# Optimization experiments

Hardware: AMD Instinct MI355X
Metric: run time of the kernel (lower is better)

## Reference

```python
import jax, jax.numpy as jnp
import numpy as np

T, H, I, E = 4096, 1024, 512, 16


def setup_inputs() -> dict:
    key = jax.random.key(0)
    k1, k2, k3 = jax.random.split(key, 3)
    x = jax.random.normal(k1, (T, H), dtype=jnp.float32)
    gate_up_proj = jax.random.normal(k2, (E, H, 2 * I), dtype=jnp.float32) * 0.02
    down_proj = jax.random.normal(k3, (E, I, H), dtype=jnp.float32) * 0.02
    # uneven expert token counts summing exactly to T (no padding rows)
    rng = np.random.default_rng(0)
    raw = rng.integers(64, 512, size=E)
    counts = (raw * T) // raw.sum()
    counts[-1] += T - counts.sum()
    num_tokens_per_expert = jnp.asarray(counts, dtype=jnp.int32)
    return {"x": x, "gate_up_proj": gate_up_proj, "down_proj": down_proj,
            "num_tokens_per_expert": num_tokens_per_expert}


def reference(x, gate_up_proj, down_proj, num_tokens_per_expert):
    # tokens are sorted by expert; build per-token expert id (jit-safe: fixed length)
    n_tok = x.shape[0]
    n_exp = gate_up_proj.shape[0]
    seg = jnp.repeat(jnp.arange(n_exp), num_tokens_per_expert, total_repeat_length=n_tok)  # [T]

    def body(acc, ew):
        e, w_gu, w_d = ew
        xe = jnp.where((seg == e)[:, None], x, jnp.zeros((), x.dtype))  # [T, H], zero rows for other experts
        gu = xe @ w_gu                                                  # [T, 2I]
        g, u = jnp.split(gu, 2, axis=-1)
        o = (jax.nn.silu(g) * u) @ w_d                                  # [T, H]; masked rows stay exactly 0
        return acc + o, None

    init = jnp.zeros((n_tok, down_proj.shape[-1]), x.dtype)
    out, _ = jax.lax.scan(body, init, (jnp.arange(n_exp), gate_up_proj, down_proj))
    return out
```

## Files before the change

### kernel.cpp

```cpp
#include <hip/hip_runtime.h>

#define H_DIM 1024
#define I_DIM 512
#define E_EXP 16
#define BM    128
#define BK    64

using bf16x8   = __attribute__((ext_vector_type(8))) short;
using floatx4  = __attribute__((ext_vector_type(4))) float;
using ushort4v = __attribute__((ext_vector_type(4))) unsigned short;

__device__ __forceinline__ unsigned short f2bf(float f) {
  union { float f; unsigned u; } v; v.f = f;
  return (unsigned short)((v.u + 0x7FFFu + ((v.u >> 16) & 1u)) >> 16);
}
__device__ __forceinline__ unsigned pk2(float a, float b) {
  return (unsigned)f2bf(a) | ((unsigned)f2bf(b) << 16);
}

__device__ __forceinline__ void gld16(const void* g, void* l) {
  __builtin_amdgcn_global_load_lds((const __attribute__((address_space(1))) void*)g,
                                   (__attribute__((address_space(3))) void*)l,
                                   16, 0, 0);
}

__device__ __forceinline__ void bar_lgkm() {
  asm volatile("s_waitcnt lgkmcnt(0)" ::: "memory");
  __builtin_amdgcn_sched_barrier(0);
  __builtin_amdgcn_s_barrier();
  __builtin_amdgcn_sched_barrier(0);
}
__device__ __forceinline__ void bar_full() {
  asm volatile("s_waitcnt vmcnt(0) lgkmcnt(0)" ::: "memory");
  __builtin_amdgcn_sched_barrier(0);
  __builtin_amdgcn_s_barrier();
  __builtin_amdgcn_sched_barrier(0);
}

__device__ __forceinline__ bool tile_info(const int* __restrict__ counts, int by,
                                          int& e, int& row0, int& base, int& cnt) {
  int acc = 0, off = 0;
  e = -1;
  #pragma unroll
  for (int i = 0; i < E_EXP; ++i) {
    int c = counts[i];
    int nt = (c + BM - 1) >> 7;
    if (e < 0 && by < acc + nt) { e = i; row0 = (by - acc) * BM; base = off; cnt = c; }
    acc += nt; off += c;
  }
  return e >= 0;
}

__global__ void k_cvt(const float* __restrict__ x, unsigned short* __restrict__ xb) {
  const float4* s4 = (const float4*)x;
  int b0 = blockIdx.x * 512 + threadIdx.x;
  float4 a = s4[b0];
  float4 b = s4[b0 + 256];
  ushort4v oa, ob;
  oa.x = f2bf(a.x); oa.y = f2bf(a.y); oa.z = f2bf(a.z); oa.w = f2bf(a.w);
  ob.x = f2bf(b.x); ob.y = f2bf(b.y); ob.z = f2bf(b.z); ob.w = f2bf(b.w);
  ((ushort4v*)xb)[b0] = oa;
  ((ushort4v*)xb)[b0 + 256] = ob;
}

__launch_bounds__(256, 4)
__global__ void k_gemm_a(const unsigned short* __restrict__ xb,
                         const float* __restrict__ wgu,
                         unsigned short* __restrict__ hb,
                         const int* __restrict__ counts) {
  __shared__ unsigned short As[2][BM * BK];
  __shared__ unsigned short Bs[64 * BK];

  int e, row0, base, cnt;
  if (!tile_info(counts, blockIdx.y, e, row0, base, cnt)) return;
  const int rows = (cnt - row0 < BM) ? (cnt - row0) : BM;
  const int c0 = blockIdx.x * 32;

  const int tid = threadIdx.x;
  const int w = tid >> 6, l = tid & 63;
  const int lr = l & 15, q = l >> 4;
  const int asr = l >> 3;
  const int akc = ((l & 7) ^ asr) * 8;
  const int cswz = lr & 7;

  const int f4  = tid & 7;
  const int seg = (tid >> 3) & 1;
  const int kb  = (tid >> 4) * 4;
  const int rb0 = seg * 32 + f4 * 4;
  const float* gptr = wgu + (size_t)e * H_DIM * (2 * I_DIM) + c0 + f4 * 4 + seg * I_DIM;
  unsigned int* BsD = (unsigned int*)Bs;
  const int cwk = kb >> 3;
  const int din = (kb >> 1) & 3;

  const int mhalf = w & 1, nhalf = w >> 1;
  const int mrow = mhalf * 64;
  const unsigned short* arow = xb + (size_t)(base + row0) * H_DIM;

  int agr[4];
  #pragma unroll
  for (int t = 0; t < 4; ++t) {
    int r = w * 32 + t * 8 + asr;
    agr[t] = (r < rows) ? r : rows - 1;
  }

  floatx4 accg[4], accu[4];
  #pragma unroll
  for (int i = 0; i < 4; ++i) { accg[i] = (floatx4){0,0,0,0}; accu[i] = (floatx4){0,0,0,0}; }

  float4 bv[4];

  auto loadB = [&](int kk) {
    #pragma unroll
    for (int j = 0; j < 4; ++j)
      bv[j] = *(const float4*)&gptr[(size_t)(kk + kb + j) * (2 * I_DIM)];
  };
  auto loadA = [&](int kk, int buf) {
    #pragma unroll
    for (int t = 0; t < 4; ++t)
      gld16(&arow[(size_t)agr[t] * H_DIM + kk + akc], &As[buf][(w * 32 + t * 8) * BK]);
  };
  auto writeB = [&]() {
    #pragma unroll
    for (int c = 0; c < 4; ++c) {
      const int r = rb0 + c;
      uint2 d;
      d.x = pk2(bv[0][c], bv[1][c]);
      d.y = pk2(bv[2][c], bv[3][c]);
      *(uint2*)&BsD[r * 32 + ((cwk ^ (r & 7)) << 2) + din] = d;
    }
  };
  auto compute = [&](int cb) {
    #pragma unroll
    for (int kf = 0; kf < 2; ++kf) {
      const int c = kf * 4 + q;
      const int ca = (c ^ cswz) * 8;
      bf16x8 af[4], bg, bu;
      #pragma unroll
      for (int mi = 0; mi < 4; ++mi)
        af[mi] = *(const bf16x8*)&As[cb][(mrow + mi * 16 + lr) * BK + ca];
      bg = *(const bf16x8*)&Bs[(nhalf * 16 + lr) * BK + ca];
      bu = *(const bf16x8*)&Bs[(32 + nhalf * 16 + lr) * BK + ca];
      #pragma unroll
      for (int mi = 0; mi < 4; ++mi) {
        accg[mi] = __builtin_amdgcn_mfma_f32_16x16x32_bf16(af[mi], bg, accg[mi], 0, 0, 0);
        accu[mi] = __builtin_amdgcn_mfma_f32_16x16x32_bf16(af[mi], bu, accu[mi], 0, 0, 0);
      }
    }
  };

  loadB(0);
  loadA(0, 0);
  writeB();
  __syncthreads();

  const int nk = H_DIM / BK;
  int cur = 0;
  for (int ki = 0; ki < nk - 1; ++ki) {
    const int kk = (ki + 1) * BK;
    loadB(kk);
    loadA(kk, cur ^ 1);
    __builtin_amdgcn_sched_barrier(0);
    compute(cur);
    bar_lgkm();
    writeB();
    bar_full();
    cur ^= 1;
  }
  compute(cur);

  #pragma unroll
  for (int mi = 0; mi < 4; ++mi)
    #pragma unroll
    for (int r = 0; r < 4; ++r) {
      int row_local = mrow + mi * 16 + q * 4 + r;
      if (row_local >= rows) continue;
      size_t orow = (size_t)(base + row0 + row_local) * I_DIM;
      float g = accg[mi][r], u = accu[mi][r];
      float s = g / (1.0f + __expf(-g)) * u;
      hb[orow + c0 + nhalf * 16 + lr] = f2bf(s);
    }
}

__launch_bounds__(256, 4)
__global__ void k_gemm_b(const unsigned short* __restrict__ hb,
                         const float* __restrict__ wdn,
                         float* __restrict__ out,
                         const int* __restrict__ counts) {
  __shared__ unsigned short As[2][BM * BK];
  __shared__ unsigned short Bs[64 * BK];

  int e, row0, base, cnt;
  if (!tile_info(counts, blockIdx.y, e, row0, base, cnt)) return;
  const int rows = (cnt - row0 < BM) ? (cnt - row0) : BM;
  const int n0 = blockIdx.x * 64;

  const int tid = threadIdx.x;
  const int w = tid >> 6, l = tid & 63;
  const int lr = l & 15, q = l >> 4;
  const int asr = l >> 3;
  const int akc = ((l & 7) ^ asr) * 8;
  const int cswz = lr & 7;

  const int f4 = tid & 15;
  const int kb = (tid >> 4) * 4;
  const int rb0 = f4 * 4;
  const float* gptr = wdn + (size_t)e * I_DIM * H_DIM + n0 + f4 * 4;
  unsigned int* BsD = (unsigned int*)Bs;
  const int cwk = kb >> 3;
  const int din = (kb >> 1) & 3;

  const int mhalf = w & 1, nhalf = w >> 1;
  const int mrow = mhalf * 64;
  const unsigned short* arow = hb + (size_t)(base + row0) * I_DIM;

  int agr[4];
  #pragma unroll
  for (int t = 0; t < 4; ++t) {
    int r = w * 32 + t * 8 + asr;
    agr[t] = (r < rows) ? r : rows - 1;
  }

  floatx4 acc[4][2];
  #pragma unroll
  for (int i = 0; i < 4; ++i)
    #pragma unroll
    for (int j = 0; j < 2; ++j) acc[i][j] = (floatx4){0,0,0,0};

  float4 bv[4];

  auto loadB = [&](int kk) {
    #pragma unroll
    for (int j = 0; j < 4; ++j)
      bv[j] = *(const float4*)&gptr[(size_t)(kk + kb + j) * H_DIM];
  };
  auto loadA = [&](int kk, int buf) {
    #pragma unroll
    for (int t = 0; t < 4; ++t)
      gld16(&arow[(size_t)agr[t] * I_DIM + kk + akc], &As[buf][(w * 32 + t * 8) * BK]);
  };
  auto writeB = [&]() {
    #pragma unroll
    for (int c = 0; c < 4; ++c) {
      const int r = rb0 + c;
      uint2 d;
      d.x = pk2(bv[0][c], bv[1][c]);
      d.y = pk2(bv[2][c], bv[3][c]);
      *(uint2*)&BsD[r * 32 + ((cwk ^ (r & 7)) << 2) + din] = d;
    }
  };
  auto compute = [&](int cb) {
    #pragma unroll
    for (int kf = 0; kf < 2; ++kf) {
      const int c = kf * 4 + q;
      const int ca = (c ^ cswz) * 8;
      bf16x8 af[4], bf[2];
      #pragma unroll
      for (int mi = 0; mi < 4; ++mi)
        af[mi] = *(const bf16x8*)&As[cb][(mrow + mi * 16 + lr) * BK + ca];
      #pragma unroll
      for (int ni = 0; ni < 2; ++ni)
        bf[ni] = *(const bf16x8*)&Bs[(nhalf * 32 + ni * 16 + lr) * BK + ca];
      #pragma unroll
      for (int mi = 0; mi < 4; ++mi)
        #pragma unroll
        for (int ni = 0; ni < 2; ++ni)
          acc[mi][ni] = __builtin_amdgcn_mfma_f32_16x16x32_bf16(af[mi], bf[ni], acc[mi][ni], 0, 0, 0);
    }
  };

  loadB(0);
  loadA(0, 0);
  writeB();
  __syncthreads();

  const int nk = I_DIM / BK;
  int cur = 0;
  for (int ki = 0; ki < nk - 1; ++ki) {
    const int kk = (ki + 1) * BK;
    loadB(kk);
    loadA(kk, cur ^ 1);
    __builtin_amdgcn_sched_barrier(0);
    compute(cur);
    bar_lgkm();
    writeB();
    bar_full();
    cur ^= 1;
  }
  compute(cur);

  #pragma unroll
  for (int mi = 0; mi < 4; ++mi)
    #pragma unroll
    for (int r = 0; r < 4; ++r) {
      int row_local = mrow + mi * 16 + q * 4 + r;
      if (row_local >= rows) continue;
      size_t orow = (size_t)(base + row0 + row_local) * H_DIM;
      #pragma unroll
      for (int ni = 0; ni < 2; ++ni)
        out[orow + n0 + nhalf * 32 + ni * 16 + lr] = acc[mi][ni][r];
    }
}

extern "C" void kernel_launch(void* const* d_in, const int* in_sizes, int n_in,
                              void* d_out, int out_size, void* d_ws, size_t ws_size,
                              hipStream_t stream) {
  const float* x      = (const float*)d_in[0];
  const float* wgu    = (const float*)d_in[1];
  const float* wdn    = (const float*)d_in[2];
  const int*   counts = (const int*)d_in[3];
  float* out = (float*)d_out;

  unsigned char* ws = (unsigned char*)d_ws;
  unsigned short* xb = (unsigned short*)(ws);
  unsigned short* hb = (unsigned short*)(ws + 8388608);

  k_cvt<<<2048, 256, 0, stream>>>(x, xb);
  k_gemm_a<<<dim3(I_DIM / 32, 48), 256, 0, stream>>>(xb, wgu, hb, counts);
  k_gemm_b<<<dim3(H_DIM / 64, 48), 256, 0, stream>>>(hb, wdn, out, counts);
}
```

Before: 170.8 us.

## Double-buffer B tiles with two-stage register prefetch and partial vmcnt waits

The B (weight) shared-memory tile is now double-buffered, and the fp32 weight loads are prefetched two K-steps ahead in registers. This lets the bf16 conversion and LDS store for the next tile happen before compute, leaving one barrier per iteration with a vmcnt(4) wait instead of two barriers with full drains. The B-tile swizzle key now also folds in row bits 3-4 to reduce LDS bank conflicts. Launch bounds drop from 4 to 3 blocks per SM to allow for the extra LDS and registers, which lowers occupancy.

```diff
diff --git a/kernel.cpp b/kernel.cpp
--- a/kernel.cpp
+++ b/kernel.cpp
@@ -6,6 +6,8 @@
 #define BM    128
 #define BK    64
 
+#define KEY(r) (((r) & 7) ^ (((r) >> 3) & 3))
+
 using bf16x8   = __attribute__((ext_vector_type(8))) short;
 using floatx4  = __attribute__((ext_vector_type(4))) float;
 using ushort4v = __attribute__((ext_vector_type(4))) unsigned short;
@@ -24,13 +26,13 @@
                                    16, 0, 0);
 }
 
-__device__ __forceinline__ void bar_lgkm() {
-  asm volatile("s_waitcnt lgkmcnt(0)" ::: "memory");
+__device__ __forceinline__ void bar_v4() {
+  asm volatile("s_waitcnt vmcnt(4) lgkmcnt(0)" ::: "memory");
   __builtin_amdgcn_sched_barrier(0);
   __builtin_amdgcn_s_barrier();
   __builtin_amdgcn_sched_barrier(0);
 }
-__device__ __forceinline__ void bar_full() {
+__device__ __forceinline__ void bar_v0() {
   asm volatile("s_waitcnt vmcnt(0) lgkmcnt(0)" ::: "memory");
   __builtin_amdgcn_sched_barrier(0);
   __builtin_amdgcn_s_barrier();
@@ -63,13 +65,13 @@
   ((ushort4v*)xb)[b0 + 256] = ob;
 }
 
-__launch_bounds__(256, 4)
+__launch_bounds__(256, 3)
 __global__ void k_gemm_a(const unsigned short* __restrict__ xb,
                          const float* __restrict__ wgu,
                          unsigned short* __restrict__ hb,
                          const int* __restrict__ counts) {
   __shared__ unsigned short As[2][BM * BK];
-  __shared__ unsigned short Bs[64 * BK];
+  __shared__ unsigned short Bs[2][64 * BK];
 
   int e, row0, base, cnt;
   if (!tile_info(counts, blockIdx.y, e, row0, base, cnt)) return;
@@ -88,7 +90,6 @@
   const int kb  = (tid >> 4) * 4;
   const int rb0 = seg * 32 + f4 * 4;
   const float* gptr = wgu + (size_t)e * H_DIM * (2 * I_DIM) + c0 + f4 * 4 + seg * I_DIM;
-  unsigned int* BsD = (unsigned int*)Bs;
   const int cwk = kb >> 3;
   const int din = (kb >> 1) & 3;
 
@@ -96,6 +97,9 @@
   const int mrow = mhalf * 64;
   const unsigned short* arow = xb + (size_t)(base + row0) * H_DIM;
 
+  const int rg = nhalf * 16 + lr;
+  const int keyB = KEY(rg);
+
   int agr[4];
   #pragma unroll
   for (int t = 0; t < 4; ++t) {
@@ -119,27 +123,29 @@
     for (int t = 0; t < 4; ++t)
       gld16(&arow[(size_t)agr[t] * H_DIM + kk + akc], &As[buf][(w * 32 + t * 8) * BK]);
   };
-  auto writeB = [&]() {
+  auto stB = [&](int buf) {
+    unsigned int* BsD = (unsigned int*)&Bs[buf][0];
     #pragma unroll
     for (int c = 0; c < 4; ++c) {
       const int r = rb0 + c;
       uint2 d;
       d.x = pk2(bv[0][c], bv[1][c]);
       d.y = pk2(bv[2][c], bv[3][c]);
-      *(uint2*)&BsD[r * 32 + ((cwk ^ (r & 7)) << 2) + din] = d;
+      *(uint2*)&BsD[r * 32 + ((cwk ^ KEY(r)) << 2) + din] = d;
     }
   };
   auto compute = [&](int cb) {
     #pragma unroll
     for (int kf = 0; kf < 2; ++kf) {
-      const int c = kf * 4 + q;
-      const int ca = (c ^ cswz) * 8;
+      const int cc = kf * 4 + q;
+      const int ca = (cc ^ cswz) * 8;
+      const int cb16 = (cc ^ keyB) * 8;
       bf16x8 af[4], bg, bu;
       #pragma unroll
       for (int mi = 0; mi < 4; ++mi)
         af[mi] = *(const bf16x8*)&As[cb][(mrow + mi * 16 + lr) * BK + ca];
-      bg = *(const bf16x8*)&Bs[(nhalf * 16 + lr) * BK + ca];
-      bu = *(const bf16x8*)&Bs[(32 + nhalf * 16 + lr) * BK + ca];
+      bg = *(const bf16x8*)&Bs[cb][rg * BK + cb16];
+      bu = *(const bf16x8*)&Bs[cb][(32 + rg) * BK + cb16];
       #pragma unroll
       for (int mi = 0; mi < 4; ++mi) {
         accg[mi] = __builtin_amdgcn_mfma_f32_16x16x32_bf16(af[mi], bg, accg[mi], 0, 0, 0);
@@ -148,22 +154,24 @@
     }
   };
 
+  const int nk = H_DIM / BK;
   loadB(0);
   loadA(0, 0);
-  writeB();
-  __syncthreads();
-
-  const int nk = H_DIM / BK;
+  stB(0);
+  loadB(BK);
+  bar_v4();
   int cur = 0;
-  for (int ki = 0; ki < nk - 1; ++ki) {
-    const int kk = (ki + 1) * BK;
-    loadB(kk);
-    loadA(kk, cur ^ 1);
+
+  for (int t = 0; t < nk - 1; ++t) {
+    loadA((t + 1) * BK, cur ^ 1);
+    stB(cur ^ 1);
+    {
+      int t2 = (t + 2 < nk) ? (t + 2) : (nk - 1);
+      loadB(t2 * BK);
+    }
     __builtin_amdgcn_sched_barrier(0);
     compute(cur);
-    bar_lgkm();
-    writeB();
-    bar_full();
+    bar_v4();
     cur ^= 1;
   }
   compute(cur);
@@ -181,13 +189,13 @@
     }
 }
 
-__launch_bounds__(256, 4)
+__launch_bounds__(256, 3)
 __global__ void k_gemm_b(const unsigned short* __restrict__ hb,
                          const float* __restrict__ wdn,
                          float* __restrict__ out,
                          const int* __restrict__ counts) {
   __shared__ unsigned short As[2][BM * BK];
-  __shared__ unsigned short Bs[64 * BK];
+  __shared__ unsigned short Bs[2][64 * BK];
 
   int e, row0, base, cnt;
   if (!tile_info(counts, blockIdx.y, e, row0, base, cnt)) return;
@@ -205,7 +213,6 @@
   const int kb = (tid >> 4) * 4;
   const int rb0 = f4 * 4;
   const float* gptr = wdn + (size_t)e * I_DIM * H_DIM + n0 + f4 * 4;
-  unsigned int* BsD = (unsigned int*)Bs;
   const int cwk = kb >> 3;
   const int din = (kb >> 1) & 3;
 
@@ -213,6 +220,10 @@
   const int mrow = mhalf * 64;
   const unsigned short* arow = hb + (size_t)(base + row0) * I_DIM;
 
+  const int rn0 = nhalf * 32 + lr;
+  const int rn1 = nhalf * 32 + 16 + lr;
+  const int key0 = KEY(rn0), key1 = KEY(rn1);
+
   int agr[4];
   #pragma unroll
   for (int t = 0; t < 4; ++t) {
@@ -238,52 +249,54 @@
     for (int t = 0; t < 4; ++t)
       gld16(&arow[(size_t)agr[t] * I_DIM + kk + akc], &As[buf][(w * 32 + t * 8) * BK]);
   };
-  auto writeB = [&]() {
+  auto stB = [&](int buf) {
+    unsigned int* BsD = (unsigned int*)&Bs[buf][0];
     #pragma unroll
     for (int c = 0; c < 4; ++c) {
       const int r = rb0 + c;
       uint2 d;
       d.x = pk2(bv[0][c], bv[1][c]);
       d.y = pk2(bv[2][c], bv[3][c]);
-      *(uint2*)&BsD[r * 32 + ((cwk ^ (r & 7)) << 2) + din] = d;
+      *(uint2*)&BsD[r * 32 + ((cwk ^ KEY(r)) << 2) + din] = d;
     }
   };
   auto compute = [&](int cb) {
     #pragma unroll
     for (int kf = 0; kf < 2; ++kf) {
-      const int c = kf * 4 + q;
-      const int ca = (c ^ cswz) * 8;
-      bf16x8 af[4], bf[2];
+      const int cc = kf * 4 + q;
+      const int ca = (cc ^ cswz) * 8;
+      bf16x8 af[4], bf0, bf1;
       #pragma unroll
       for (int mi = 0; mi < 4; ++mi)
         af[mi] = *(const bf16x8*)&As[cb][(mrow + mi * 16 + lr) * BK + ca];
-      #pragma unroll
-      for (int ni = 0; ni < 2; ++ni)
-        bf[ni] = *(const bf16x8*)&Bs[(nhalf * 32 + ni * 16 + lr) * BK + ca];
-      #pragma unroll
-      for (int mi = 0; mi < 4; ++mi)
-        #pragma unroll
-        for (int ni = 0; ni < 2; ++ni)
-          acc[mi][ni] = __builtin_amdgcn_mfma_f32_16x16x32_bf16(af[mi], bf[ni], acc[mi][ni], 0, 0, 0);
-    }
-  };
-
+      bf0 = *(const bf16x8*)&Bs[cb][rn0 * BK + (cc ^ key0) * 8];
+      bf1 = *(const bf16x8*)&Bs[cb][rn1 * BK + (cc ^ key1) * 8];
+      #pragma unroll
+      for (int mi = 0; mi < 4; ++mi) {
+        acc[mi][0] = __builtin_amdgcn_mfma_f32_16x16x32_bf16(af[mi], bf0, acc[mi][0], 0, 0, 0);
+        acc[mi][1] = __builtin_amdgcn_mfma_f32_16x16x32_bf16(af[mi], bf1, acc[mi][1], 0, 0, 0);
+      }
+    }
+  };
+
+  const int nk = I_DIM / BK;
   loadB(0);
   loadA(0, 0);
-  writeB();
-  __syncthreads();
-
-  const int nk = I_DIM / BK;
+  stB(0);
+  loadB(BK);
+  bar_v4();
   int cur = 0;
-  for (int ki = 0; ki < nk - 1; ++ki) {
-    const int kk = (ki + 1) * BK;
-    loadB(kk);
-    loadA(kk, cur ^ 1);
+
+  for (int t = 0; t < nk - 1; ++t) {
+    loadA((t + 1) * BK, cur ^ 1);
+    stB(cur ^ 1);
+    {
+      int t2 = (t + 2 < nk) ? (t + 2) : (nk - 1);
+      loadB(t2 * BK);
+    }
     __builtin_amdgcn_sched_barrier(0);
     compute(cur);
-    bar_lgkm();
-    writeB();
-    bar_full();
+    bar_v4();
     cur ^= 1;
   }
   compute(cur);
```

Result: no change. 172.5 us (+1.0%).
